# Kernel tuning notes

Measured on AMD Instinct MI355X. Metric: run time of the kernel, lower is better.

The kernel has to match this reference:

```python
import jax, jax.numpy as jnp
import numpy as np

NEG_SLOPE = 0.2  # PyG GATConv default leaky_relu slope


def gat_conv(x_src, x_dst, src, dst, Ws, Wd, a_s, a_d, bias, n_dst, heads, ch,
             concat, edge_w=None, We=None, a_e=None):
    """PyG-style GATConv (bipartite, add_self_loops=False, eval mode)."""
    hs = (x_src @ Ws).reshape(-1, heads, ch)   # [Ns,H,C]
    hd = (x_dst @ Wd).reshape(-1, heads, ch)   # [Nd,H,C]
    a_src = jnp.einsum('nhc,hc->nh', hs, a_s)  # [Ns,H]
    a_dst = jnp.einsum('nhc,hc->nh', hd, a_d)  # [Nd,H]
    logits = a_src[src] + a_dst[dst]           # [E,H]
    if edge_w is not None:
        he = (edge_w[:, None] @ We).reshape(-1, heads, ch)  # lin_edge proj
        logits = logits + jnp.einsum('ehc,hc->eh', he, a_e)
    logits = jax.nn.leaky_relu(logits, NEG_SLOPE)
    # segment softmax grouped by destination node
    m = jax.ops.segment_max(logits, dst, num_segments=n_dst)
    e = jnp.exp(logits - m[dst])
    denom = jax.ops.segment_sum(e, dst, num_segments=n_dst)
    alpha = e / denom[dst]                     # [E,H]
    out = jax.ops.segment_sum(hs[src] * alpha[..., None], dst, num_segments=n_dst)
    out = out.reshape(n_dst, heads * ch) if concat else out.mean(axis=1)
    return out + bias


def setup_inputs() -> dict:
    key = jax.random.key(0)
    ks = jax.random.split(key, 40)
    NA = NB = 50000
    F = 128
    E = 800000
    HID = 100
    d = {}
    d['x_A'] = jax.random.normal(ks[0], (NA, F), jnp.float32)
    d['x_B'] = jax.random.normal(ks[1], (NB, F), jnp.float32)
    d['ei_AB'] = jax.random.randint(ks[2], (2, E), 0, NA)  # row0=src in A, row1=dst in B
    d['ei_BA'] = jax.random.randint(ks[3], (2, E), 0, NB)
    d['w_AB'] = jax.random.uniform(ks[4], (E,), jnp.float32)
    d['w_BA'] = jax.random.uniform(ks[5], (E,), jnp.float32)
    idx = [6]
    def p(shape):
        v = jax.random.normal(ks[idx[0]], shape, jnp.float32) * 0.1
        idx[0] += 1
        return v
    for et in ('AB', 'BA'):
        d['l1_%s_Ws' % et] = p((F, HID)); d['l1_%s_Wd' % et] = p((F, HID))
        d['l1_%s_as' % et] = p((4, 25)); d['l1_%s_ad' % et] = p((4, 25))
        d['l1_%s_We' % et] = p((1, HID)); d['l1_%s_ae' % et] = p((4, 25))
        d['l1_%s_b' % et] = p((HID,))
        d['l2_%s_Ws' % et] = p((HID, HID)); d['l2_%s_Wd' % et] = p((HID, HID))
        d['l2_%s_as' % et] = p((1, HID)); d['l2_%s_ad' % et] = p((1, HID))
        d['l2_%s_b' % et] = p((HID,))
    return d


def reference(x_A, x_B, ei_AB, ei_BA, w_AB, w_BA,
              l1_AB_Ws, l1_AB_Wd, l1_AB_as, l1_AB_ad, l1_AB_We, l1_AB_ae, l1_AB_b,
              l1_BA_Ws, l1_BA_Wd, l1_BA_as, l1_BA_ad, l1_BA_We, l1_BA_ae, l1_BA_b,
              l2_AB_Ws, l2_AB_Wd, l2_AB_as, l2_AB_ad, l2_AB_b,
              l2_BA_Ws, l2_BA_Wd, l2_BA_as, l2_BA_ad, l2_BA_b):
    NA, NB = x_A.shape[0], x_B.shape[0]
    s_ab, d_ab = ei_AB[0], ei_AB[1]
    s_ba, d_ba = ei_BA[0], ei_BA[1]
    # layer 1: heads=4, out=25 per head, concat -> 100, edge_dim=1
    hB = gat_conv(x_A, x_B, s_ab, d_ab, l1_AB_Ws, l1_AB_Wd, l1_AB_as, l1_AB_ad,
                  l1_AB_b, NB, 4, 25, True, w_AB, l1_AB_We, l1_AB_ae)
    hA = gat_conv(x_B, x_A, s_ba, d_ba, l1_BA_Ws, l1_BA_Wd, l1_BA_as, l1_BA_ad,
                  l1_BA_b, NA, 4, 25, True, w_BA, l1_BA_We, l1_BA_ae)
    # dropout is identity in eval mode
    hA = jax.nn.elu(hA)
    hB = jax.nn.elu(hB)
    # layer 2: heads=1, out=100, concat=False (mean over 1 head), no edge_dim
    oB = gat_conv(hA, hB, s_ab, d_ab, l2_AB_Ws, l2_AB_Wd, l2_AB_as, l2_AB_ad,
                  l2_AB_b, NB, 1, 100, False)
    oA = gat_conv(hB, hA, s_ba, d_ba, l2_BA_Ws, l2_BA_Wd, l2_BA_as, l2_BA_ad,
                  l2_BA_b, NA, 1, 100, False)
    return jnp.stack([oA, oB])  # [2, 50000, 100]
```

## Files before the change

kernel.cpp:

```cpp
#include <hip/hip_runtime.h>


#define NNODES 50000
#define NEDGES 800000
#define SCAN_T 1024
#define SCAN_NBLK ((NNODES + SCAN_T - 1) / SCAN_T)

typedef unsigned short u16;
typedef unsigned int u32;

__device__ __forceinline__ float b2f(u16 u) {
    union { u32 i; float f; } x;
    x.i = ((u32)u) << 16;
    return x.f;
}
__device__ __forceinline__ u16 f2b(float f) {
    union { float f; u32 i; } x;
    x.f = f;
    u32 r = x.i + 0x7FFFu + ((x.i >> 16) & 1u);
    return (u16)(r >> 16);
}

__global__ void ce_kernel(const float* __restrict__ WeA, const float* __restrict__ aeA,
                          const float* __restrict__ WeB, const float* __restrict__ aeB,
                          float* __restrict__ ce ) {
    const float* We = blockIdx.x ? WeB : WeA;
    const float* ae = blockIdx.x ? aeB : aeA;
    __shared__ float s[4];
    int tid = threadIdx.x;
    if (tid < 4) s[tid] = 0.f;
    __syncthreads();
    if (tid < 100) atomicAdd(&s[tid / 25], We[tid] * ae[tid]);
    __syncthreads();
    if (tid < 4) ce[blockIdx.x * 4 + tid] = s[tid];
}

__global__ void count_kernel(const int* __restrict__ eiA, const int* __restrict__ eiB,
                             int E, int* cntA, int* cntB) {
    int i = blockIdx.x * blockDim.x + threadIdx.x;
    if (i < E) atomicAdd(&cntA[eiA[E + i]], 1);
    else if (i < 2 * E) atomicAdd(&cntB[eiB[E + (i - E)]], 1);
}

__global__ __launch_bounds__(SCAN_T) void scanA_kernel(
    const int* __restrict__ cntA, const int* __restrict__ cntB,
    int* __restrict__ roA, int* __restrict__ roB, int* __restrict__ partial, int N) {
    const int dir = blockIdx.y;
    const int* cnt = dir ? cntB : cntA;
    int* ro = dir ? roB : roA;
    const int tid = threadIdx.x;
    const int i = blockIdx.x * SCAN_T + tid;
    __shared__ int sm[SCAN_T];
    sm[tid] = (i < N) ? cnt[i] : 0;
    __syncthreads();
    for (int off = 1; off < SCAN_T; off <<= 1) {
        int t = (tid >= off) ? sm[tid - off] : 0;
        __syncthreads();
        sm[tid] += t;
        __syncthreads();
    }
    if (i < N) ro[i + 1] = sm[tid];
    if (tid == SCAN_T - 1) partial[dir * 64 + blockIdx.x] = sm[tid];
}

__global__ void scanB_kernel(int* __restrict__ partial, int nblk) {
    __shared__ int sm[128];
    const int tid = threadIdx.x;
    sm[tid] = ((tid & 63) < nblk) ? partial[tid] : 0;
    __syncthreads();
    if (tid < 2) {
        int run = 0;
        for (int b = 0; b < nblk; ++b) {
            int t = sm[tid * 64 + b];
            sm[tid * 64 + b] = run;
            run += t;
        }
    }
    __syncthreads();
    partial[tid] = sm[tid];
}

__global__ __launch_bounds__(SCAN_T) void scanC_kernel(
    const int* __restrict__ cntA, const int* __restrict__ cntB,
    int* __restrict__ roA, int* __restrict__ roB,
    int* __restrict__ curA, int* __restrict__ curB,
    const int* __restrict__ partial, int N) {
    const int dir = blockIdx.y;
    const int* cnt = dir ? cntB : cntA;
    int* ro = dir ? roB : roA;
    int* cur = dir ? curB : curA;
    const int poff = partial[dir * 64 + blockIdx.x];
    const int i = blockIdx.x * SCAN_T + threadIdx.x;
    if (i < N) {
        int c = cnt[i];
        int r = ro[i + 1] + poff;
        ro[i + 1] = r;
        cur[i] = r - c;
        if (i == 0) ro[0] = 0;
    }
}

__global__ void fill_kernel(const int* __restrict__ eiA, const int* __restrict__ eiB,
                            const float* __restrict__ wA, const float* __restrict__ wB,
                            int E, int* curA, int* curB,
                            int* __restrict__ ssA, int* __restrict__ ssB,
                            float* __restrict__ swA, float* __restrict__ swB) {
    int i = blockIdx.x * blockDim.x + threadIdx.x;
    if (i < E) {
        int s = eiA[i], d = eiA[E + i];
        int pos = atomicAdd(&curA[d], 1);
        ssA[pos] = s; swA[pos] = wA[i];
    } else if (i < 2 * E) {
        int j = i - E;
        int s = eiB[j], d = eiB[E + j];
        int pos = atomicAdd(&curB[d], 1);
        ssB[pos] = s; swB[pos] = wB[j];
    }
}

struct GemmArgs {
    const float* X;
    const float* W;
    const float* a;
    void* H;
    float* att;
};

template <int K, int HEADS>
__global__ __launch_bounds__(256, 2) void gemm_att_kernel(
    GemmArgs g0, GemmArgs g1, GemmArgs g2, GemmArgs g3, int N) {
    const GemmArgs ga[4] = {g0, g1, g2, g3};
    const GemmArgs g = ga[blockIdx.y];
    constexpr int XS_STRIDE = 33;
    constexpr int XS_BUF = 128 * XS_STRIDE;
    constexpr int WS_STRIDE = 28;
    constexpr int WS_WAVE = 32 * WS_STRIDE;
    constexpr int WS_BUF = 4 * WS_WAVE;
    constexpr int SMEM_BYTES = (2 * XS_BUF + 2 * WS_BUF) * 4;
    __shared__ __align__(16) char smem[SMEM_BYTES];
    const int tid = threadIdx.x;
    const int lane = tid & 63;
    const int w = tid >> 6;
    const int node0 = blockIdx.x * 128;
    const int nA = node0 + lane;
    const int nB = node0 + 64 + lane;
    const bool vA = nA < N, vB = nB < N;

    const int c0 = __builtin_amdgcn_readfirstlane(25 * w);

    float acc0[25], acc1[25];
#pragma unroll
    for (int j = 0; j < 25; ++j) { acc0[j] = 0.f; acc1[j] = 0.f; }

    float* Xs = (float*)smem;
    float* Wsh = (float*)smem + 2 * XS_BUF;
    float4 rv[4];
    float wv[13];

    auto issue_x = [&](int k0) {
#pragma unroll
        for (int r = 0; r < 4; ++r) {
            const int s = tid + r * 256;
            const int n = s >> 3;
            const int ko = (s & 7) * 4;
            int row = node0 + n;
            if (row >= N) row = N - 1;
            const float* xp = g.X + (size_t)row * K + k0 + ko;
            if constexpr (K % 32 == 0) {
                rv[r] = *(const float4*)xp;
            } else {
                const int kb = k0 + ko;
                float4 v = make_float4(0.f, 0.f, 0.f, 0.f);
                if (kb + 3 < K) {
                    v = *(const float4*)xp;
                } else {
                    if (kb < K) v.x = xp[0];
                    if (kb + 1 < K) v.y = xp[1];
                    if (kb + 2 < K) v.z = xp[2];
                }
                rv[r] = v;
            }
        }
    };
    auto write_x = [&](int buf) {
#pragma unroll
        for (int r = 0; r < 4; ++r) {
            const int s = tid + r * 256;
            const int n = s >> 3;
            const int ko = (s & 7) * 4;
            float* dst = Xs + buf * XS_BUF + n * XS_STRIDE + ko;
            dst[0] = rv[r].x;
            dst[1] = rv[r].y;
            dst[2] = rv[r].z;
            dst[3] = rv[r].w;
        }
    };
    auto issue_w = [&](int k0, int kc) {
        const int lim = kc * 100;
#pragma unroll
        for (int r = 0; r < 13; ++r) {
            const int e = tid + r * 256;
            wv[r] = (e < lim) ? g.W[(size_t)k0 * 100 + e] : 0.f;
        }
    };
    auto write_w = [&](int buf, int kc) {
        const int lim = kc * 100;
#pragma unroll
        for (int r = 0; r < 13; ++r) {
            const int e = tid + r * 256;
            if (e < lim) {
                const int k = e / 100;
                const int j = e - k * 100;
                const int hd = j / 25;
                const int jj = j - hd * 25;
                Wsh[buf * WS_BUF + hd * WS_WAVE + k * WS_STRIDE + jj] = wv[r];
            }
        }
    };

    constexpr int C = (K + 31) / 32;
    {
        const int kc0 = (K < 32) ? K : 32;
        issue_x(0);
        issue_w(0, kc0);
        write_x(0);
        write_w(0, kc0);
    }
    __syncthreads();
    for (int c = 0; c < C; ++c) {
        const int k0 = c * 32;
        const int kc = (K - k0 < 32) ? (K - k0) : 32;
        const int kcn = (K - k0 - 32 < 32) ? (K - k0 - 32) : 32;
        if (c + 1 < C) {
            issue_x(k0 + 32);
            issue_w(k0 + 32, kcn);
        }
        const float* x0p = Xs + (c & 1) * XS_BUF + lane * XS_STRIDE;
        const float* x1p = x0p + 64 * XS_STRIDE;
        const float* wp = Wsh + (c & 1) * WS_BUF + w * WS_WAVE;
#pragma unroll 4
        for (int kk = 0; kk < kc; ++kk) {
            const float xs0 = x0p[kk];
            const float xs1 = x1p[kk];
            float wr[25];
#pragma unroll
            for (int j = 0; j < 25; ++j) wr[j] = wp[kk * WS_STRIDE + j];
#pragma unroll
            for (int j = 0; j < 25; ++j) {
                acc0[j] = fmaf(xs0, wr[j], acc0[j]);
                acc1[j] = fmaf(xs1, wr[j], acc1[j]);
            }
        }
        if (c + 1 < C) {
            __syncthreads();
            write_x((c + 1) & 1);
            write_w((c + 1) & 1, kcn);
        }
        __syncthreads();
    }

    float ap0 = 0.f, ap1 = 0.f;
#pragma unroll
    for (int j = 0; j < 25; ++j) {
        const float av = g.a[c0 + j];
        ap0 = fmaf(acc0[j], av, ap0);
        ap1 = fmaf(acc1[j], av, ap1);
    }

    const int rem = N - node0;
    if (HEADS == 4) {
        if (g.H == nullptr) {
            if (vA) g.att[(size_t)nA * 4 + w] = ap0;
            if (vB) g.att[(size_t)nB * 4 + w] = ap1;
        } else {
            u16* sh = (u16*)smem;
            u32* sh32 = (u32*)smem;
#pragma unroll
            for (int j = 0; j < 25; ++j) sh[lane * 106 + c0 + j] = f2b(acc0[j]);
            sh[lane * 106 + 100 + w] = f2b(ap0);
            __syncthreads();
            {
                const int limA = ((rem < 64) ? rem : 64) * 52;
                u32* Hb = (u32*)g.H + (size_t)node0 * 64;
                for (int i = tid; i < 64 * 52; i += 256) {
                    if (i < limA) {
                        int nd = i / 52;
                        int off = i - nd * 52;
                        Hb[nd * 64 + off] = sh32[nd * 53 + off];
                    }
                }
            }
            __syncthreads();
#pragma unroll
            for (int j = 0; j < 25; ++j) sh[lane * 106 + c0 + j] = f2b(acc1[j]);
            sh[lane * 106 + 100 + w] = f2b(ap1);
            __syncthreads();
            {
                const int remB = rem - 64;
                const int limB = ((remB < 64) ? (remB < 0 ? 0 : remB) : 64) * 52;
                u32* Hb = (u32*)g.H + (size_t)(node0 + 64) * 64;
                for (int i = tid; i < 64 * 52; i += 256) {
                    if (i < limB) {
                        int nd = i / 52;
                        int off = i - nd * 52;
                        Hb[nd * 64 + off] = sh32[nd * 53 + off];
                    }
                }
            }
        }
    } else {
        u16* sh = (u16*)smem;
        u32* sh32 = (u32*)smem;
        float* attp = (float*)(smem + 64 * 102 * 2);
        attp[w * 128 + lane] = ap0;
        attp[w * 128 + 64 + lane] = ap1;
        if (g.H != nullptr) {
#pragma unroll
            for (int j = 0; j < 25; ++j) sh[lane * 102 + c0 + j] = f2b(acc0[j]);
            __syncthreads();
            {
                const int limA = ((rem < 64) ? rem : 64) * 50;
                u32* Hb = (u32*)g.H + (size_t)node0 * 64;
                for (int i = tid; i < 64 * 50; i += 256) {
                    if (i < limA) {
                        int nd = i / 50;
                        int off = i - nd * 50;
                        Hb[nd * 64 + off] = sh32[nd * 51 + off];
                    }
                }
                if (tid < 128 && node0 + tid < N)
                    g.att[node0 + tid] =
                        attp[tid] + attp[128 + tid] + attp[256 + tid] + attp[384 + tid];
            }
            __syncthreads();
#pragma unroll
            for (int j = 0; j < 25; ++j) sh[lane * 102 + c0 + j] = f2b(acc1[j]);
            __syncthreads();
            {
                const int remB = rem - 64;
                const int limB = ((remB < 64) ? (remB < 0 ? 0 : remB) : 64) * 50;
                u32* Hb = (u32*)g.H + (size_t)(node0 + 64) * 64;
                for (int i = tid; i < 64 * 50; i += 256) {
                    if (i < limB) {
                        int nd = i / 50;
                        int off = i - nd * 50;
                        Hb[nd * 64 + off] = sh32[nd * 51 + off];
                    }
                }
            }
        } else {
            __syncthreads();
            if (tid < 128 && node0 + tid < N)
                g.att[node0 + tid] =
                    attp[tid] + attp[128 + tid] + attp[256 + tid] + attp[384 + tid];
        }
    }
}

struct Gather4Args {
    const int* ro;
    const int* ss;
    const float* sw;
    const u16* hp;
    const float* ad;
    const float* ce;
    const float* bias;
    float* outp;
};

__global__ __launch_bounds__(256) void gather4_kernel(Gather4Args ga0, Gather4Args ga1, int Nd) {
    const Gather4Args ga[2] = {ga0, ga1};
    const Gather4Args g = ga[blockIdx.y];
    int wid = (int)((blockIdx.x * blockDim.x + threadIdx.x) >> 6);
    if (wid >= Nd) return;
    const int n = __builtin_amdgcn_readfirstlane(wid);
    const int lane = threadIdx.x & 63;
    const int beg = g.ro[n], end = g.ro[n + 1];
    const bool act = (lane < 50);
    const int cc0 = act ? 2 * lane : 0;
    const int h0 = cc0 / 25;
    const int h1 = (cc0 + 1) / 25;
    const int aoff = 2 * (h0 >> 1);
    const float ce0 = g.ce[h0], ce1 = g.ce[h1];
    const float ad0 = g.ad[n * 4 + h0], ad1 = g.ad[n * 4 + h1];
    float acc0 = 0.f, acc1 = 0.f, d0 = 0.f, d1 = 0.f;

    auto edge = [&](u32 va, u32 aa, float wq, float& p0o, float& p1o) {
        const float as0 = b2f((h0 & 1) ? (u16)(aa >> 16) : (u16)aa);
        const float as1 = b2f((h1 & 1) ? (u16)(aa >> 16) : (u16)aa);
        float l0 = as0 + ad0 + wq * ce0;
        float l1 = as1 + ad1 + wq * ce1;
        l0 = fmaxf(l0, 0.2f * l0);
        l1 = fmaxf(l1, 0.2f * l1);
        const float p0 = __expf(l0);
        const float p1 = __expf(l1);
        acc0 = fmaf(p0, b2f((u16)va), acc0);
        acc1 = fmaf(p1, b2f((u16)(va >> 16)), acc1);
        p0o = p0;
        p1o = p1;
    };

    struct G4 { u32 va0, aa0, va1, aa1, va2, aa2, va3, aa3; float w0, w1, w2, w3; };
    auto load4 = [&](int off) -> G4 {
        G4 r;
        const int o = __builtin_amdgcn_readfirstlane(off);
        const int s0 = g.ss[o];
        const int s1 = g.ss[o + 1];
        const int s2 = g.ss[o + 2];
        const int s3 = g.ss[o + 3];
        r.w0 = g.sw[o];
        r.w1 = g.sw[o + 1];
        r.w2 = g.sw[o + 2];
        r.w3 = g.sw[o + 3];
        const u16* r0 = g.hp + (size_t)s0 * 128;
        const u16* r1 = g.hp + (size_t)s1 * 128;
        const u16* r2 = g.hp + (size_t)s2 * 128;
        const u16* r3 = g.hp + (size_t)s3 * 128;
        r.va0 = *(const u32*)(r0 + cc0);
        r.aa0 = *(const u32*)(r0 + 100 + aoff);
        r.va1 = *(const u32*)(r1 + cc0);
        r.aa1 = *(const u32*)(r1 + 100 + aoff);
        r.va2 = *(const u32*)(r2 + cc0);
        r.aa2 = *(const u32*)(r2 + 100 + aoff);
        r.va3 = *(const u32*)(r3 + cc0);
        r.aa3 = *(const u32*)(r3 + 100 + aoff);
        return r;
    };
    auto compute4 = [&](const G4& e) {
        float pa0, pa1, pb0, pb1;
        edge(e.va0, e.aa0, e.w0, pa0, pa1);
        edge(e.va1, e.aa1, e.w1, pb0, pb1);
        d0 += pa0 + pb0;
        d1 += pa1 + pb1;
        edge(e.va2, e.aa2, e.w2, pa0, pa1);
        edge(e.va3, e.aa3, e.w3, pb0, pb1);
        d0 += pa0 + pb0;
        d1 += pa1 + pb1;
    };

    int i = beg;
    const int last4 = beg + ((end - beg) & ~3);
    const int ng = (last4 - beg) >> 2;
    if (ng >= 2) {
        G4 cur = load4(i);
        G4 nxt = load4(i + 4);
        i += 8;
        for (; i < last4; i += 4) {
            G4 nn = load4(i);
            __builtin_amdgcn_sched_barrier(0);
            compute4(cur);
            cur = nxt;
            nxt = nn;
        }
        compute4(cur);
        compute4(nxt);
    } else if (ng == 1) {
        G4 cur = load4(i);
        compute4(cur);
        i += 4;
    }
    if (i + 1 < end) {
        const int o = __builtin_amdgcn_readfirstlane(i);
        const int s0 = g.ss[o], s1 = g.ss[o + 1];
        const float w0 = g.sw[o], w1 = g.sw[o + 1];
        const u16* r0 = g.hp + (size_t)s0 * 128;
        const u16* r1 = g.hp + (size_t)s1 * 128;
        const u32 va0 = *(const u32*)(r0 + cc0);
        const u32 aa0 = *(const u32*)(r0 + 100 + aoff);
        const u32 va1 = *(const u32*)(r1 + cc0);
        const u32 aa1 = *(const u32*)(r1 + 100 + aoff);
        float pa0, pa1, pb0, pb1;
        edge(va0, aa0, w0, pa0, pa1);
        edge(va1, aa1, w1, pb0, pb1);
        d0 += pa0 + pb0;
        d1 += pa1 + pb1;
        i += 2;
    }
    if (i < end) {
        const int o = __builtin_amdgcn_readfirstlane(i);
        const int s0 = g.ss[o];
        const float w0 = g.sw[o];
        const u16* r0 = g.hp + (size_t)s0 * 128;
        const u32 va0 = *(const u32*)(r0 + cc0);
        const u32 aa0 = *(const u32*)(r0 + 100 + aoff);
        float pa0, pa1;
        edge(va0, aa0, w0, pa0, pa1);
        d0 += pa0;
        d1 += pa1;
    }

    if (act) {
        float r0 = (end > beg) ? acc0 / d0 : 0.f;
        float r1 = (end > beg) ? acc1 / d1 : 0.f;
        r0 += g.bias[cc0];
        r0 = (r0 > 0.f) ? r0 : (__expf(r0) - 1.f);
        r1 += g.bias[cc0 + 1];
        r1 = (r1 > 0.f) ? r1 : (__expf(r1) - 1.f);
        *(float2*)(g.outp + (size_t)n * 100 + cc0) = make_float2(r0, r1);
    }
}

struct Gather1Args {
    const int* ro;
    const int* ss;
    const u16* hp;
    const float* as_;
    const float* ad;
    const float* bias;
    float* outp;
};

__global__ __launch_bounds__(256) void gather1_kernel(Gather1Args ga0, Gather1Args ga1, int Nd) {
    const Gather1Args ga[2] = {ga0, ga1};
    const Gather1Args g = ga[blockIdx.y];
    int wid = (int)((blockIdx.x * blockDim.x + threadIdx.x) >> 6);
    if (wid >= Nd) return;
    const int n = __builtin_amdgcn_readfirstlane(wid);
    const int lane = threadIdx.x & 63;
    const int beg = g.ro[n], end = g.ro[n + 1];
    const bool act = (lane < 50);
    const int cc0 = act ? 2 * lane : 0;
    const float adn = g.ad[n];
    float acc0 = 0.f, acc1 = 0.f, d0 = 0.f;

    auto edge = [&](u32 va, float asq, float& po) {
        float l = asq + adn;
        l = fmaxf(l, 0.2f * l);
        const float p = __expf(l);
        acc0 = fmaf(p, b2f((u16)va), acc0);
        acc1 = fmaf(p, b2f((u16)(va >> 16)), acc1);
        po = p;
    };

    struct G1 { u32 va0, va1, va2, va3; float a0, a1, a2, a3; };
    auto load4 = [&](int off) -> G1 {
        G1 r;
        const int o = __builtin_amdgcn_readfirstlane(off);
        const int s0 = g.ss[o];
        const int s1 = g.ss[o + 1];
        const int s2 = g.ss[o + 2];
        const int s3 = g.ss[o + 3];
        r.a0 = g.as_[s0];
        r.a1 = g.as_[s1];
        r.a2 = g.as_[s2];
        r.a3 = g.as_[s3];
        r.va0 = *(const u32*)(g.hp + (size_t)s0 * 128 + cc0);
        r.va1 = *(const u32*)(g.hp + (size_t)s1 * 128 + cc0);
        r.va2 = *(const u32*)(g.hp + (size_t)s2 * 128 + cc0);
        r.va3 = *(const u32*)(g.hp + (size_t)s3 * 128 + cc0);
        return r;
    };
    auto compute4 = [&](const G1& e) {
        float pa, pb;
        edge(e.va0, e.a0, pa);
        edge(e.va1, e.a1, pb);
        d0 += pa + pb;
        edge(e.va2, e.a2, pa);
        edge(e.va3, e.a3, pb);
        d0 += pa + pb;
    };

    int i = beg;
    const int last4 = beg + ((end - beg) & ~3);
    const int ng = (last4 - beg) >> 2;
    if (ng >= 2) {
        G1 cur = load4(i);
        G1 nxt = load4(i + 4);
        i += 8;
        for (; i < last4; i += 4) {
            G1 nn = load4(i);
            __builtin_amdgcn_sched_barrier(0);
            compute4(cur);
            cur = nxt;
            nxt = nn;
        }
        compute4(cur);
        compute4(nxt);
    } else if (ng == 1) {
        G1 cur = load4(i);
        compute4(cur);
        i += 4;
    }
    if (i + 1 < end) {
        const int o = __builtin_amdgcn_readfirstlane(i);
        const int s0 = g.ss[o], s1 = g.ss[o + 1];
        const float a0 = g.as_[s0], a1 = g.as_[s1];
        const u32 va0 = *(const u32*)(g.hp + (size_t)s0 * 128 + cc0);
        const u32 va1 = *(const u32*)(g.hp + (size_t)s1 * 128 + cc0);
        float pa, pb;
        edge(va0, a0, pa);
        edge(va1, a1, pb);
        d0 += pa + pb;
        i += 2;
    }
    if (i < end) {
        const int o = __builtin_amdgcn_readfirstlane(i);
        const int s0 = g.ss[o];
        const float a0 = g.as_[s0];
        const u32 va0 = *(const u32*)(g.hp + (size_t)s0 * 128 + cc0);
        float pa;
        edge(va0, a0, pa);
        d0 += pa;
    }

    if (act) {
        float r0 = (end > beg) ? acc0 / d0 : 0.f;
        float r1 = (end > beg) ? acc1 / d0 : 0.f;
        r0 += g.bias[cc0];
        r1 += g.bias[cc0 + 1];
        *(float2*)(g.outp + (size_t)n * 100 + cc0) = make_float2(r0, r1);
    }
}

extern "C" void kernel_launch(void* const* d_in, const int* in_sizes, int n_in,
                              void* d_out, int out_size, void* d_ws, size_t ws_size,
                              hipStream_t stream) {
    const float* x_A   = (const float*)d_in[0];
    const float* x_B   = (const float*)d_in[1];
    const int*   ei_AB = (const int*)d_in[2];
    const int*   ei_BA = (const int*)d_in[3];
    const float* w_AB  = (const float*)d_in[4];
    const float* w_BA  = (const float*)d_in[5];
    const float* l1AB_Ws = (const float*)d_in[6];
    const float* l1AB_Wd = (const float*)d_in[7];
    const float* l1AB_as = (const float*)d_in[8];
    const float* l1AB_ad = (const float*)d_in[9];
    const float* l1AB_We = (const float*)d_in[10];
    const float* l1AB_ae = (const float*)d_in[11];
    const float* l1AB_b  = (const float*)d_in[12];
    const float* l2AB_Ws = (const float*)d_in[13];
    const float* l2AB_Wd = (const float*)d_in[14];
    const float* l2AB_as = (const float*)d_in[15];
    const float* l2AB_ad = (const float*)d_in[16];
    const float* l2AB_b  = (const float*)d_in[17];
    const float* l1BA_Ws = (const float*)d_in[18];
    const float* l1BA_Wd = (const float*)d_in[19];
    const float* l1BA_as = (const float*)d_in[20];
    const float* l1BA_ad = (const float*)d_in[21];
    const float* l1BA_We = (const float*)d_in[22];
    const float* l1BA_ae = (const float*)d_in[23];
    const float* l1BA_b  = (const float*)d_in[24];
    const float* l2BA_Ws = (const float*)d_in[25];
    const float* l2BA_Wd = (const float*)d_in[26];
    const float* l2BA_as = (const float*)d_in[27];
    const float* l2BA_ad = (const float*)d_in[28];
    const float* l2BA_b  = (const float*)d_in[29];

    const int N = NNODES, E = NEDGES;

    size_t o = 0;
    auto alloc = [&](size_t n) { size_t r = o; o += (n + 63) & ~(size_t)63; return r; };
    size_t cntA = alloc(N), cntB = alloc(N);
    size_t roA = alloc(N + 1), roB = alloc(N + 1);
    size_t curA = alloc(N), curB = alloc(N);
    size_t ssA = alloc(E), ssB = alloc(E);
    size_t swA = alloc(E), swB = alloc(E);
    size_t ce8 = alloc(8);
    size_t part = alloc(128);
    size_t pHAB = alloc((size_t)N * 64);
    size_t pHBA = alloc((size_t)N * 64);
    size_t ad1B = alloc((size_t)N * 4), ad1A = alloc((size_t)N * 4);
    size_t hA1 = alloc((size_t)N * 100), hB1 = alloc((size_t)N * 100);
    size_t H2AB = alloc((size_t)N * 64);
    size_t H2BA = alloc((size_t)N * 64);
    size_t as2AB = alloc(N), as2BA = alloc(N);
    size_t ad2AB = alloc(N), ad2BA = alloc(N);
    (void)ws_size;

    float* wsf = (float*)d_ws;
    int*   wsi = (int*)d_ws;
    u32*   wsu = (u32*)d_ws;

    hipMemsetAsync(wsi + cntA, 0, sizeof(int) * (cntB + N - cntA), stream);

    ce_kernel<<<2, 128, 0, stream>>>(l1AB_We, l1AB_ae, l1BA_We, l1BA_ae, wsf + ce8);

    const int eb = (2 * E + 255) / 256;
    count_kernel<<<eb, 256, 0, stream>>>(ei_AB, ei_BA, E, wsi + cntA, wsi + cntB);
    scanA_kernel<<<dim3(SCAN_NBLK, 2), SCAN_T, 0, stream>>>(
        wsi + cntA, wsi + cntB, wsi + roA, wsi + roB, wsi + part, N);
    scanB_kernel<<<1, 128, 0, stream>>>(wsi + part, SCAN_NBLK);
    scanC_kernel<<<dim3(SCAN_NBLK, 2), SCAN_T, 0, stream>>>(
        wsi + cntA, wsi + cntB, wsi + roA, wsi + roB, wsi + curA, wsi + curB, wsi + part, N);
    fill_kernel<<<eb, 256, 0, stream>>>(ei_AB, ei_BA, w_AB, w_BA, E, wsi + curA, wsi + curB,
                                        wsi + ssA, wsi + ssB, wsf + swA, wsf + swB);

    const int gb = (N + 127) / 128;
    {
        GemmArgs g0 = {x_A, l1AB_Ws, l1AB_as, (void*)(wsu + pHAB), nullptr};
        GemmArgs g1 = {x_B, l1AB_Wd, l1AB_ad, nullptr, wsf + ad1B};
        GemmArgs g2 = {x_B, l1BA_Ws, l1BA_as, (void*)(wsu + pHBA), nullptr};
        GemmArgs g3 = {x_A, l1BA_Wd, l1BA_ad, nullptr, wsf + ad1A};
        gemm_att_kernel<128, 4><<<dim3(gb, 4), 256, 0, stream>>>(g0, g1, g2, g3, N);
    }

    const int wb = (N + 3) / 4;
    {
        Gather4Args g0 = {wsi + roA, wsi + ssA, wsf + swA, (const u16*)(wsu + pHAB),
                          wsf + ad1B, wsf + ce8, l1AB_b, wsf + hB1};
        Gather4Args g1 = {wsi + roB, wsi + ssB, wsf + swB, (const u16*)(wsu + pHBA),
                          wsf + ad1A, wsf + ce8 + 4, l1BA_b, wsf + hA1};
        gather4_kernel<<<dim3(wb, 2), 256, 0, stream>>>(g0, g1, N);
    }

    {
        GemmArgs g0 = {wsf + hA1, l2AB_Ws, l2AB_as, (void*)(wsu + H2AB), wsf + as2AB};
        GemmArgs g1 = {wsf + hB1, l2AB_Wd, l2AB_ad, nullptr, wsf + ad2AB};
        GemmArgs g2 = {wsf + hB1, l2BA_Ws, l2BA_as, (void*)(wsu + H2BA), wsf + as2BA};
        GemmArgs g3 = {wsf + hA1, l2BA_Wd, l2BA_ad, nullptr, wsf + ad2BA};
        gemm_att_kernel<100, 1><<<dim3(gb, 4), 256, 0, stream>>>(g0, g1, g2, g3, N);
    }

    float* out = (float*)d_out;
    {
        Gather1Args g0 = {wsi + roA, wsi + ssA, (const u16*)(wsu + H2AB), wsf + as2AB,
                          wsf + ad2AB, l2AB_b, out + (size_t)N * 100};
        Gather1Args g1 = {wsi + roB, wsi + ssB, (const u16*)(wsu + H2BA), wsf + as2BA,
                          wsf + ad2BA, l2BA_b, out};
        gather1_kernel<<<dim3(wb, 2), 256, 0, stream>>>(g0, g1, N);
    }
}
```

Baseline: 921.2 us.

## Precompute per-edge attention exponentials in separate edge kernels before gathers

Adds edge-parallel kernels that compute leaky-relu plus exp attention weights once per edge (four heads in layer 1, one in layer 2) and store them in CSR order. This needs a sorted destination array from the fill kernel and a source-attention output from the GEMM. The gather kernels then read the precomputed weights instead of recomputing exp redundantly across lanes and loading per-source attention values. The cost is extra global traffic for the edge-weight arrays and two more kernel launches.

```diff
diff --git a/kernel.cpp b/kernel.cpp
--- a/kernel.cpp
+++ b/kernel.cpp
@@ -104,17 +104,18 @@
                             const float* __restrict__ wA, const float* __restrict__ wB,
                             int E, int* curA, int* curB,
                             int* __restrict__ ssA, int* __restrict__ ssB,
+                            int* __restrict__ sdA, int* __restrict__ sdB,
                             float* __restrict__ swA, float* __restrict__ swB) {
     int i = blockIdx.x * blockDim.x + threadIdx.x;
     if (i < E) {
         int s = eiA[i], d = eiA[E + i];
         int pos = atomicAdd(&curA[d], 1);
-        ssA[pos] = s; swA[pos] = wA[i];
+        ssA[pos] = s; sdA[pos] = d; swA[pos] = wA[i];
     } else if (i < 2 * E) {
         int j = i - E;
         int s = eiB[j], d = eiB[E + j];
         int pos = atomicAdd(&curB[d], 1);
-        ssB[pos] = s; swB[pos] = wB[j];
+        ssB[pos] = s; sdB[pos] = d; swB[pos] = wB[j];
     }
 }
 
@@ -269,10 +270,13 @@
 
     const int rem = N - node0;
     if (HEADS == 4) {
-        if (g.H == nullptr) {
-            if (vA) g.att[(size_t)nA * 4 + w] = ap0;
-            if (vB) g.att[(size_t)nB * 4 + w] = ap1;
-        } else {
+        if (g.att != nullptr) {
+            const float w0 = (g.H != nullptr) ? b2f(f2b(ap0)) : ap0;
+            const float w1 = (g.H != nullptr) ? b2f(f2b(ap1)) : ap1;
+            if (vA) g.att[(size_t)nA * 4 + w] = w0;
+            if (vB) g.att[(size_t)nB * 4 + w] = w1;
+        }
+        if (g.H != nullptr) {
             u16* sh = (u16*)smem;
             u32* sh32 = (u32*)smem;
 #pragma unroll
@@ -357,13 +361,58 @@
     }
 }
 
+struct EdgeP4Args {
+    const int* ss;
+    const int* sd;
+    const float* sw;
+    const float* aS;
+    const float* aD;
+    const float* ce;
+    float* p4;
+};
+
+__global__ void edge_p4_kernel(EdgeP4Args a0, EdgeP4Args a1, int E) {
+    const EdgeP4Args a = blockIdx.y ? a1 : a0;
+    const int e = blockIdx.x * 256 + threadIdx.x;
+    if (e >= E) return;
+    const int s = a.ss[e];
+    const int d = a.sd[e];
+    const float w = a.sw[e];
+    const float4 as4 = *(const float4*)(a.aS + (size_t)s * 4);
+    const float4 ad4 = *(const float4*)(a.aD + (size_t)d * 4);
+    float4 p;
+    float l;
+    l = as4.x + ad4.x + w * a.ce[0]; l = fmaxf(l, 0.2f * l); p.x = __expf(l);
+    l = as4.y + ad4.y + w * a.ce[1]; l = fmaxf(l, 0.2f * l); p.y = __expf(l);
+    l = as4.z + ad4.z + w * a.ce[2]; l = fmaxf(l, 0.2f * l); p.z = __expf(l);
+    l = as4.w + ad4.w + w * a.ce[3]; l = fmaxf(l, 0.2f * l); p.w = __expf(l);
+    *(float4*)(a.p4 + (size_t)e * 4) = p;
+}
+
+struct EdgeP1Args {
+    const int* ss;
+    const int* sd;
+    const float* aS;
+    const float* aD;
+    float* p1;
+};
+
+__global__ void edge_p1_kernel(EdgeP1Args a0, EdgeP1Args a1, int E) {
+    const EdgeP1Args a = blockIdx.y ? a1 : a0;
+    const int e = blockIdx.x * 256 + threadIdx.x;
+    if (e >= E) return;
+    const int s = a.ss[e];
+    const int d = a.sd[e];
+    float l = a.aS[s] + a.aD[d];
+    l = fmaxf(l, 0.2f * l);
+    a.p1[e] = __expf(l);
+}
+
 struct Gather4Args {
     const int* ro;
     const int* ss;
-    const float* sw;
     const u16* hp;
-    const float* ad;
-    const float* ce;
+    const float* p4;
     const float* bias;
     float* outp;
 };
@@ -381,26 +430,18 @@
     const int h0 = cc0 / 25;
     const int h1 = (cc0 + 1) / 25;
     const int aoff = 2 * (h0 >> 1);
-    const float ce0 = g.ce[h0], ce1 = g.ce[h1];
-    const float ad0 = g.ad[n * 4 + h0], ad1 = g.ad[n * 4 + h1];
     float acc0 = 0.f, acc1 = 0.f, d0 = 0.f, d1 = 0.f;
 
-    auto edge = [&](u32 va, u32 aa, float wq, float& p0o, float& p1o) {
-        const float as0 = b2f((h0 & 1) ? (u16)(aa >> 16) : (u16)aa);
-        const float as1 = b2f((h1 & 1) ? (u16)(aa >> 16) : (u16)aa);
-        float l0 = as0 + ad0 + wq * ce0;
-        float l1 = as1 + ad1 + wq * ce1;
-        l0 = fmaxf(l0, 0.2f * l0);
-        l1 = fmaxf(l1, 0.2f * l1);
-        const float p0 = __expf(l0);
-        const float p1 = __expf(l1);
+    auto edge = [&](u32 va, float2 pp, float& p0o, float& p1o) {
+        const float p0 = (h0 & 1) ? pp.y : pp.x;
+        const float p1 = (h1 & 1) ? pp.y : pp.x;
         acc0 = fmaf(p0, b2f((u16)va), acc0);
         acc1 = fmaf(p1, b2f((u16)(va >> 16)), acc1);
         p0o = p0;
         p1o = p1;
     };
 
-    struct G4 { u32 va0, aa0, va1, aa1, va2, aa2, va3, aa3; float w0, w1, w2, w3; };
+    struct G4 { u32 va0, va1, va2, va3; float2 pp0, pp1, pp2, pp3; };
     auto load4 = [&](int off) -> G4 {
         G4 r;
         const int o = __builtin_amdgcn_readfirstlane(off);
@@ -408,32 +449,24 @@
         const int s1 = g.ss[o + 1];
         const int s2 = g.ss[o + 2];
         const int s3 = g.ss[o + 3];
-        r.w0 = g.sw[o];
-        r.w1 = g.sw[o + 1];
-        r.w2 = g.sw[o + 2];
-        r.w3 = g.sw[o + 3];
-        const u16* r0 = g.hp + (size_t)s0 * 128;
-        const u16* r1 = g.hp + (size_t)s1 * 128;
-        const u16* r2 = g.hp + (size_t)s2 * 128;
-        const u16* r3 = g.hp + (size_t)s3 * 128;
-        r.va0 = *(const u32*)(r0 + cc0);
-        r.aa0 = *(const u32*)(r0 + 100 + aoff);
-        r.va1 = *(const u32*)(r1 + cc0);
-        r.aa1 = *(const u32*)(r1 + 100 + aoff);
-        r.va2 = *(const u32*)(r2 + cc0);
-        r.aa2 = *(const u32*)(r2 + 100 + aoff);
-        r.va3 = *(const u32*)(r3 + cc0);
-        r.aa3 = *(const u32*)(r3 + 100 + aoff);
+        r.pp0 = *(const float2*)(g.p4 + (size_t)o * 4 + aoff);
+        r.pp1 = *(const float2*)(g.p4 + (size_t)(o + 1) * 4 + aoff);
+        r.pp2 = *(const float2*)(g.p4 + (size_t)(o + 2) * 4 + aoff);
+        r.pp3 = *(const float2*)(g.p4 + (size_t)(o + 3) * 4 + aoff);
+        r.va0 = *(const u32*)(g.hp + (size_t)s0 * 128 + cc0);
+        r.va1 = *(const u32*)(g.hp + (size_t)s1 * 128 + cc0);
+        r.va2 = *(const u32*)(g.hp + (size_t)s2 * 128 + cc0);
+        r.va3 = *(const u32*)(g.hp + (size_t)s3 * 128 + cc0);
         return r;
     };
     auto compute4 = [&](const G4& e) {
         float pa0, pa1, pb0, pb1;
-        edge(e.va0, e.aa0, e.w0, pa0, pa1);
-        edge(e.va1, e.aa1, e.w1, pb0, pb1);
+        edge(e.va0, e.pp0, pa0, pa1);
+        edge(e.va1, e.pp1, pb0, pb1);
         d0 += pa0 + pb0;
         d1 += pa1 + pb1;
-        edge(e.va2, e.aa2, e.w2, pa0, pa1);
-        edge(e.va3, e.aa3, e.w3, pb0, pb1);
+        edge(e.va2, e.pp2, pa0, pa1);
+        edge(e.va3, e.pp3, pb0, pb1);
         d0 += pa0 + pb0;
         d1 += pa1 + pb1;
     };
@@ -462,16 +495,13 @@
     if (i + 1 < end) {
         const int o = __builtin_amdgcn_readfirstlane(i);
         const int s0 = g.ss[o], s1 = g.ss[o + 1];
-        const float w0 = g.sw[o], w1 = g.sw[o + 1];
-        const u16* r0 = g.hp + (size_t)s0 * 128;
-        const u16* r1 = g.hp + (size_t)s1 * 128;
-        const u32 va0 = *(const u32*)(r0 + cc0);
-        const u32 aa0 = *(const u32*)(r0 + 100 + aoff);
-        const u32 va1 = *(const u32*)(r1 + cc0);
-        const u32 aa1 = *(const u32*)(r1 + 100 + aoff);
+        const float2 pp0 = *(const float2*)(g.p4 + (size_t)o * 4 + aoff);
+        const float2 pp1 = *(const float2*)(g.p4 + (size_t)(o + 1) * 4 + aoff);
+        const u32 va0 = *(const u32*)(g.hp + (size_t)s0 * 128 + cc0);
+        const u32 va1 = *(const u32*)(g.hp + (size_t)s1 * 128 + cc0);
         float pa0, pa1, pb0, pb1;
-        edge(va0, aa0, w0, pa0, pa1);
-        edge(va1, aa1, w1, pb0, pb1);
+        edge(va0, pp0, pa0, pa1);
+        edge(va1, pp1, pb0, pb1);
         d0 += pa0 + pb0;
         d1 += pa1 + pb1;
         i += 2;
@@ -479,12 +509,10 @@
     if (i < end) {
         const int o = __builtin_amdgcn_readfirstlane(i);
         const int s0 = g.ss[o];
-        const float w0 = g.sw[o];
-        const u16* r0 = g.hp + (size_t)s0 * 128;
-        const u32 va0 = *(const u32*)(r0 + cc0);
-        const u32 aa0 = *(const u32*)(r0 + 100 + aoff);
+        const float2 pp0 = *(const float2*)(g.p4 + (size_t)o * 4 + aoff);
+        const u32 va0 = *(const u32*)(g.hp + (size_t)s0 * 128 + cc0);
         float pa0, pa1;
-        edge(va0, aa0, w0, pa0, pa1);
+        edge(va0, pp0, pa0, pa1);
         d0 += pa0;
         d1 += pa1;
     }
@@ -504,8 +532,7 @@
     const int* ro;
     const int* ss;
     const u16* hp;
-    const float* as_;
-    const float* ad;
+    const float* p1;
     const float* bias;
     float* outp;
 };
@@ -520,19 +547,14 @@
     const int beg = g.ro[n], end = g.ro[n + 1];
     const bool act = (lane < 50);
     const int cc0 = act ? 2 * lane : 0;
-    const float adn = g.ad[n];
     float acc0 = 0.f, acc1 = 0.f, d0 = 0.f;
 
-    auto edge = [&](u32 va, float asq, float& po) {
-        float l = asq + adn;
-        l = fmaxf(l, 0.2f * l);
-        const float p = __expf(l);
+    auto edge = [&](u32 va, float p) {
         acc0 = fmaf(p, b2f((u16)va), acc0);
         acc1 = fmaf(p, b2f((u16)(va >> 16)), acc1);
-        po = p;
-    };
-
-    struct G1 { u32 va0, va1, va2, va3; float a0, a1, a2, a3; };
+    };
+
+    struct G1 { u32 va0, va1, va2, va3; float p0, p1, p2, p3; };
     auto load4 = [&](int off) -> G1 {
         G1 r;
         const int o = __builtin_amdgcn_readfirstlane(off);
@@ -540,10 +562,10 @@
         const int s1 = g.ss[o + 1];
         const int s2 = g.ss[o + 2];
         const int s3 = g.ss[o + 3];
-        r.a0 = g.as_[s0];
-        r.a1 = g.as_[s1];
-        r.a2 = g.as_[s2];
-        r.a3 = g.as_[s3];
+        r.p0 = g.p1[o];
+        r.p1 = g.p1[o + 1];
+        r.p2 = g.p1[o + 2];
+        r.p3 = g.p1[o + 3];
         r.va0 = *(const u32*)(g.hp + (size_t)s0 * 128 + cc0);
         r.va1 = *(const u32*)(g.hp + (size_t)s1 * 128 + cc0);
         r.va2 = *(const u32*)(g.hp + (size_t)s2 * 128 + cc0);
@@ -551,13 +573,12 @@
         return r;
     };
     auto compute4 = [&](const G1& e) {
-        float pa, pb;
-        edge(e.va0, e.a0, pa);
-        edge(e.va1, e.a1, pb);
-        d0 += pa + pb;
-        edge(e.va2, e.a2, pa);
-        edge(e.va3, e.a3, pb);
-        d0 += pa + pb;
+        edge(e.va0, e.p0);
+        edge(e.va1, e.p1);
+        d0 += e.p0 + e.p1;
+        edge(e.va2, e.p2);
+        edge(e.va3, e.p3);
+        d0 += e.p2 + e.p3;
     };
 
     int i = beg;
@@ -584,23 +605,21 @@
     if (i + 1 < end) {
         const int o = __builtin_amdgcn_readfirstlane(i);
         const int s0 = g.ss[o], s1 = g.ss[o + 1];
-        const float a0 = g.as_[s0], a1 = g.as_[s1];
+        const float p0 = g.p1[o], p1v = g.p1[o + 1];
         const u32 va0 = *(const u32*)(g.hp + (size_t)s0 * 128 + cc0);
         const u32 va1 = *(const u32*)(g.hp + (size_t)s1 * 128 + cc0);
-        float pa, pb;
-        edge(va0, a0, pa);
-        edge(va1, a1, pb);
-        d0 += pa + pb;
+        edge(va0, p0);
+        edge(va1, p1v);
+        d0 += p0 + p1v;
         i += 2;
     }
     if (i < end) {
         const int o = __builtin_amdgcn_readfirstlane(i);
         const int s0 = g.ss[o];
-        const float a0 = g.as_[s0];
+        const float p0 = g.p1[o];
         const u32 va0 = *(const u32*)(g.hp + (size_t)s0 * 128 + cc0);
-        float pa;
-        edge(va0, a0, pa);
-        d0 += pa;
+        edge(va0, p0);
+        d0 += p0;
     }
 
     if (act) {
@@ -654,17 +673,21 @@
     size_t roA = alloc(N + 1), roB = alloc(N + 1);
     size_t curA = alloc(N), curB = alloc(N);
     size_t ssA = alloc(E), ssB = alloc(E);
+    size_t sdA = alloc(E), sdB = alloc(E);
     size_t swA = alloc(E), swB = alloc(E);
     size_t ce8 = alloc(8);
     size_t part = alloc(128);
     size_t pHAB = alloc((size_t)N * 64);
     size_t pHBA = alloc((size_t)N * 64);
     size_t ad1B = alloc((size_t)N * 4), ad1A = alloc((size_t)N * 4);
+    size_t aS1AB = alloc((size_t)N * 4), aS1BA = alloc((size_t)N * 4);
+    size_t p4AB = alloc((size_t)E * 4), p4BA = alloc((size_t)E * 4);
     size_t hA1 = alloc((size_t)N * 100), hB1 = alloc((size_t)N * 100);
     size_t H2AB = alloc((size_t)N * 64);
     size_t H2BA = alloc((size_t)N * 64);
     size_t as2AB = alloc(N), as2BA = alloc(N);
     size_t ad2AB = alloc(N), ad2BA = alloc(N);
+    size_t p1AB = alloc(E), p1BA = alloc(E);
     (void)ws_size;
 
     float* wsf = (float*)d_ws;
@@ -676,6 +699,7 @@
     ce_kernel<<<2, 128, 0, stream>>>(l1AB_We, l1AB_ae, l1BA_We, l1BA_ae, wsf + ce8);
 
     const int eb = (2 * E + 255) / 256;
+    const int eb1 = (E + 255) / 256;
     count_kernel<<<eb, 256, 0, stream>>>(ei_AB, ei_BA, E, wsi + cntA, wsi + cntB);
     scanA_kernel<<<dim3(SCAN_NBLK, 2), SCAN_T, 0, stream>>>(
         wsi + cntA, wsi + cntB, wsi + roA, wsi + roB, wsi + part, N);
@@ -683,23 +707,32 @@
     scanC_kernel<<<dim3(SCAN_NBLK, 2), SCAN_T, 0, stream>>>(
         wsi + cntA, wsi + cntB, wsi + roA, wsi + roB, wsi + curA, wsi + curB, wsi + part, N);
     fill_kernel<<<eb, 256, 0, stream>>>(ei_AB, ei_BA, w_AB, w_BA, E, wsi + curA, wsi + curB,
-                                        wsi + ssA, wsi + ssB, wsf + swA, wsf + swB);
+                                        wsi + ssA, wsi + ssB, wsi + sdA, wsi + sdB,
+                                        wsf + swA, wsf + swB);
 
     const int gb = (N + 127) / 128;
     {
-        GemmArgs g0 = {x_A, l1AB_Ws, l1AB_as, (void*)(wsu + pHAB), nullptr};
+        GemmArgs g0 = {x_A, l1AB_Ws, l1AB_as, (void*)(wsu + pHAB), wsf + aS1AB};
         GemmArgs g1 = {x_B, l1AB_Wd, l1AB_ad, nullptr, wsf + ad1B};
-        GemmArgs g2 = {x_B, l1BA_Ws, l1BA_as, (void*)(wsu + pHBA), nullptr};
+        GemmArgs g2 = {x_B, l1BA_Ws, l1BA_as, (void*)(wsu + pHBA), wsf + aS1BA};
         GemmArgs g3 = {x_A, l1BA_Wd, l1BA_ad, nullptr, wsf + ad1A};
         gemm_att_kernel<128, 4><<<dim3(gb, 4), 256, 0, stream>>>(g0, g1, g2, g3, N);
     }
 
+    {
+        EdgeP4Args a0 = {wsi + ssA, wsi + sdA, wsf + swA, wsf + aS1AB, wsf + ad1B,
+                         wsf + ce8, wsf + p4AB};
+        EdgeP4Args a1 = {wsi + ssB, wsi + sdB, wsf + swB, wsf + aS1BA, wsf + ad1A,
+                         wsf + ce8 + 4, wsf + p4BA};
+        edge_p4_kernel<<<dim3(eb1, 2), 256, 0, stream>>>(a0, a1, E);
+    }
+
     const int wb = (N + 3) / 4;
     {
-        Gather4Args g0 = {wsi + roA, wsi + ssA, wsf + swA, (const u16*)(wsu + pHAB),
-                          wsf + ad1B, wsf + ce8, l1AB_b, wsf + hB1};
-        Gather4Args g1 = {wsi + roB, wsi + ssB, wsf + swB, (const u16*)(wsu + pHBA),
-                          wsf + ad1A, wsf + ce8 + 4, l1BA_b, wsf + hA1};
+        Gather4Args g0 = {wsi + roA, wsi + ssA, (const u16*)(wsu + pHAB), wsf + p4AB,
+                          l1AB_b, wsf + hB1};
+        Gather4Args g1 = {wsi + roB, wsi + ssB, (const u16*)(wsu + pHBA), wsf + p4BA,
+                          l1BA_b, wsf + hA1};
         gather4_kernel<<<dim3(wb, 2), 256, 0, stream>>>(g0, g1, N);
     }
 
@@ -711,12 +744,18 @@
         gemm_att_kernel<100, 1><<<dim3(gb, 4), 256, 0, stream>>>(g0, g1, g2, g3, N);
     }
 
+    {
+        EdgeP1Args a0 = {wsi + ssA, wsi + sdA, wsf + as2AB, wsf + ad2AB, wsf + p1AB};
+        EdgeP1Args a1 = {wsi + ssB, wsi + sdB, wsf + as2BA, wsf + ad2BA, wsf + p1BA};
+        edge_p1_kernel<<<dim3(eb1, 2), 256, 0, stream>>>(a0, a1, E);
+    }
+
     float* out = (float*)d_out;
     {
-        Gather1Args g0 = {wsi + roA, wsi + ssA, (const u16*)(wsu + H2AB), wsf + as2AB,
-                          wsf + ad2AB, l2AB_b, out + (size_t)N * 100};
-        Gather1Args g1 = {wsi + roB, wsi + ssB, (const u16*)(wsu + H2BA), wsf + as2BA,
-                          wsf + ad2BA, l2BA_b, out};
+        Gather1Args g0 = {wsi + roA, wsi + ssA, (const u16*)(wsu + H2AB), wsf + p1AB,
+                          l2AB_b, out + (size_t)N * 100};
+        Gather1Args g1 = {wsi + roB, wsi + ssB, (const u16*)(wsu + H2BA), wsf + p1BA,
+                          l2BA_b, out};
         gather1_kernel<<<dim3(wb, 2), 256, 0, stream>>>(g0, g1, N);
     }
 }
```

After: 928.0 us. Within noise of the previous version (+0.7%).
